# Kernel optimization log

Measured on AMD Instinct MI355X. Metric: run time of the kernel, lower is better.

The kernel has to match this reference:

```python
import jax, jax.numpy as jnp
import numpy as np

N_CODEBOOKS = 9
CODEBOOK_SIZE = 1024
CODEBOOK_DIM = 8
INPUT_DIM = 128
B, T = 16, 4096


def setup_inputs() -> dict:
    key = jax.random.key(0)
    ks = jax.random.split(key, 7)
    x = jax.random.normal(ks[0], (B, 2 * INPUT_DIM, T), dtype=jnp.float32)
    noise = jax.random.normal(ks[1], (B, INPUT_DIM, T), dtype=jnp.float32)
    # per-codebook params (stacked over the quantizer axis)
    in_w = jax.random.normal(ks[2], (N_CODEBOOKS, CODEBOOK_DIM, INPUT_DIM), dtype=jnp.float32) * 0.08
    in_b = jax.random.normal(ks[3], (N_CODEBOOKS, CODEBOOK_DIM), dtype=jnp.float32) * 0.01
    codebook = jax.random.normal(ks[4], (N_CODEBOOKS, CODEBOOK_SIZE, CODEBOOK_DIM), dtype=jnp.float32)
    out_w = jax.random.normal(ks[5], (N_CODEBOOKS, INPUT_DIM, CODEBOOK_DIM), dtype=jnp.float32) * 0.08
    out_b = jax.random.normal(ks[6], (N_CODEBOOKS, INPUT_DIM), dtype=jnp.float32) * 0.01
    return {"x": x, "noise": noise, "in_w": in_w, "in_b": in_b,
            "codebook": codebook, "out_w": out_w, "out_b": out_b}


def _l2norm(v, eps=1e-12):
    n = jnp.linalg.norm(v, axis=-1, keepdims=True)
    return v / jnp.maximum(n, eps)


def reference(x, noise, in_w, in_b, codebook, out_w, out_b):
    # --- vae_sample ---
    mean, scale = jnp.split(x, 2, axis=1)
    stdev = jax.nn.softplus(scale) + 1e-4
    var = stdev * stdev
    kl = jnp.mean(jnp.sum(mean * mean + var - jnp.log(var) - 1.0, axis=1))
    z = noise * stdev + mean  # [B, D, T]

    # --- ResidualVectorQuantize (eval mode, all codebooks) ---
    residual = z
    z_q = jnp.zeros_like(z)
    commitment_loss = jnp.float32(0.0)
    codebook_loss = jnp.float32(0.0)
    codes, lats = [], []
    b, _, t = z.shape
    for i in range(N_CODEBOOKS):
        # in_proj (1x1 conv)
        z_e = jnp.einsum("cd,bdt->bct", in_w[i], residual) + in_b[i][None, :, None]
        enc = z_e.transpose(0, 2, 1).reshape(b * t, CODEBOOK_DIM)
        enc_n = _l2norm(enc)
        cb_n = _l2norm(codebook[i])
        # squared L2 distance between normalized vectors
        dist = (jnp.sum(enc_n * enc_n, axis=1, keepdims=True)
                - 2.0 * enc_n @ cb_n.T
                + jnp.sum(cb_n * cb_n, axis=1)[None, :])
        idx = jnp.argmin(dist, axis=1).reshape(b, t)  # [B, T]
        zq_i = codebook[i][idx].transpose(0, 2, 1)  # [B, c, T] (raw codebook)
        # mse_loss(...).mean([1,2]).mean() == global mean
        commitment_loss = commitment_loss + jnp.mean((z_e - jax.lax.stop_gradient(zq_i)) ** 2)
        codebook_loss = codebook_loss + jnp.mean((zq_i - jax.lax.stop_gradient(z_e)) ** 2)
        # straight-through estimator
        zq_st = z_e + jax.lax.stop_gradient(zq_i - z_e)
        out = jnp.einsum("dc,bct->bdt", out_w[i], zq_st) + out_b[i][None, :, None]
        z_q = z_q + out
        residual = residual - out
        codes.append(idx)
        lats.append(z_e)
    codes = jnp.stack(codes, axis=1)          # [B, N, T]
    latents = jnp.concatenate(lats, axis=1)   # [B, N*c, T]
    commitment_loss = commitment_loss / N_CODEBOOKS
    codebook_loss = codebook_loss / N_CODEBOOKS
    return z_q, kl, commitment_loss, codebook_loss, codes, latents
```

## Files before the change

kernel.cpp:

```cpp
#include <hip/hip_runtime.h>
#include <cstdint>
#include <cstddef>

constexpr int T   = 4096;
constexpr int BB  = 16;
constexpr int D   = 128;
constexpr int CB  = 1024;
constexpr int CD  = 8;
constexpr int NCB = 9;

constexpr int TBLK = 64;
constexpr int NTHR = 512;
constexpr int NW   = 8;
constexpr int ZLS  = 66;

constexpr size_t OFF_ZQ    = 0;
constexpr size_t OFF_SCAL  = (size_t)BB * D * T;
constexpr size_t OFF_CODES = OFF_SCAL + 3;
constexpr size_t OFF_LAT   = OFF_CODES + (size_t)BB * NCB * T;

constexpr size_t AFR_U32 = (size_t)NCB * 64 * 2 * 64 * 4;
constexpr size_t H2C_F32 = (size_t)NCB * CB;
constexpr size_t AFW_U32 = (size_t)2 * 6 * 2 * 5 * 64 * 4;
constexpr size_t CM_F32  = (size_t)NCB * 72 * 8;
constexpr size_t OBS_F32 = 128;
constexpr size_t BEF_F32 = 72;
constexpr size_t OP_F32  = (size_t)NCB * CB * D;

typedef short bf16x8 __attribute__((ext_vector_type(8)));
typedef float f32x4  __attribute__((ext_vector_type(4)));

__device__ __forceinline__ unsigned short f2bf(float f) {
    unsigned u = __float_as_uint(f);
    return (unsigned short)((u + (((u >> 16) & 1u) + 0x7FFFu)) >> 16);
}
__device__ __forceinline__ float bf2f(unsigned short b) {
    return __uint_as_float((unsigned)b << 16);
}

constexpr int PAIR_A[6] = {0, 0, 1, 1, 2, 0};
constexpr int PAIR_B[6] = {0, 1, 0, 1, 0, 2};

__device__ __forceinline__ unsigned short splitterm(float xv, int term) {
    unsigned short t0 = f2bf(xv); if (term == 0) return t0;
    float r1 = xv - bf2f(t0);
    unsigned short t1 = f2bf(r1); if (term == 1) return t1;
    float r2 = r1 - bf2f(t1);
    return f2bf(r2);
}

__global__ void prep_kernel(const float* __restrict__ codebook,
                            const float* __restrict__ in_w,
                            const float* __restrict__ in_b,
                            const float* __restrict__ out_w,
                            const float* __restrict__ out_b,
                            unsigned* __restrict__ afr,
                            float* __restrict__ h2c,
                            unsigned* __restrict__ afw,
                            float* __restrict__ CMt,
                            float* __restrict__ obs,
                            float* __restrict__ bef,
                            float* __restrict__ OPt,
                            float* __restrict__ scal) {
    const int gid = blockIdx.x * blockDim.x + threadIdx.x;
    if (gid == 0) { scal[0] = 0.f; scal[1] = 0.f; scal[2] = 0.f; }

    if (gid < NCB * CB) {
        const int e  = gid;
        const int i  = e >> 10;
        const int en = e & 1023;
        const int et = en >> 4;
        const int m  = en & 15;

        float v[CD]; float s2 = 0.f;
#pragma unroll
        for (int j = 0; j < CD; ++j) { v[j] = codebook[(size_t)e * CD + j]; s2 = fmaf(v[j], v[j], s2); }
        float inv = 1.0f / fmaxf(sqrtf(s2), 1e-12f);
        float cn[CD]; float c2 = 0.f;
#pragma unroll
        for (int j = 0; j < CD; ++j) { cn[j] = v[j] * inv; c2 = fmaf(cn[j], cn[j], c2); }
        h2c[e] = -0.5f * c2;

        unsigned pk[3][4];
#pragma unroll
        for (int w = 0; w < 4; ++w) {
            float x0 = cn[2 * w], x1 = cn[2 * w + 1];
            unsigned short a0 = f2bf(x0); float r0 = x0 - bf2f(a0);
            unsigned short a1 = f2bf(r0); float q0 = r0 - bf2f(a1);
            unsigned short a2 = f2bf(q0);
            unsigned short b0 = f2bf(x1); float r1 = x1 - bf2f(b0);
            unsigned short b1 = f2bf(r1); float q1 = r1 - bf2f(b1);
            unsigned short b2 = f2bf(q1);
            pk[0][w] = (unsigned)a0 | ((unsigned)b0 << 16);
            pk[1][w] = (unsigned)a1 | ((unsigned)b1 << 16);
            pk[2][w] = (unsigned)a2 | ((unsigned)b2 << 16);
        }
        const int At[8] = {0, 1, 2, 0, 1, 0, 2, 1};
#pragma unroll
        for (int kh = 0; kh < 2; ++kh) {
#pragma unroll
            for (int h = 0; h < 4; ++h) {
                int A1 = At[kh * 4 + (h >> 1)];
                int A2 = At[kh * 4 + 2 + (h >> 1)];
                int dw = (h & 1) * 2;
                size_t off = ((((size_t)i * 64 + et) * 2 + kh) * 64 + (h * 16 + m)) * 4;
                afr[off + 0] = pk[A1][dw];
                afr[off + 1] = pk[A1][dw + 1];
                afr[off + 2] = pk[A2][dw];
                afr[off + 3] = pk[A2][dw + 1];
            }
        }
        return;
    }
    if (gid < 2 * NCB * CB) {
        const int e = gid - NCB * CB;
        const int i = e >> 10;
        float cv[CD];
#pragma unroll
        for (int d = 0; d < CD; ++d) cv[d] = codebook[(size_t)e * CD + d];
        const float* ow = out_w + (size_t)i * D * CD;
        float* dst = OPt + (size_t)e * D;
        for (int r = 0; r < D; ++r) {
            float a = 0.f;
#pragma unroll
            for (int d = 0; d < CD; ++d) a = fmaf(ow[r * CD + d], cv[d], a);
            dst[r] = a;
        }
        return;
    }
    if (gid < 2 * NCB * CB + NCB * 72) {
        const int idx = gid - 2 * NCB * CB;
        const int j = idx / 72, r = idx - j * 72;
        const float* wi = in_w + (size_t)r * D;
        const float* ow = out_w + (size_t)j * D * CD;
        float a[CD];
#pragma unroll
        for (int d = 0; d < CD; ++d) a[d] = 0.f;
        for (int k = 0; k < D; ++k) {
            float w = wi[k];
#pragma unroll
            for (int d = 0; d < CD; ++d) a[d] = fmaf(w, ow[k * CD + d], a[d]);
        }
#pragma unroll
        for (int d = 0; d < CD; ++d) CMt[((size_t)j * 72 + r) * CD + d] = a[d];
        return;
    }
    if (gid < 2 * NCB * CB + NCB * 72 + 128) {
        const int r = gid - (2 * NCB * CB + NCB * 72);
        float a = 0.f;
        for (int i = 0; i < NCB; ++i) a += out_b[(size_t)i * D + r];
        obs[r] = a;
        return;
    }
    if (gid < 2 * NCB * CB + NCB * 72 + 128 + 72) {
        const int row = gid - (2 * NCB * CB + NCB * 72 + 128);
        const int ic  = row >> 3;
        const float* wi = in_w + (size_t)row * D;
        float a = in_b[row];
        for (int j = 0; j < ic; ++j) {
            const float* ob = out_b + (size_t)j * D;
            float s = 0.f;
            for (int k = 0; k < D; ++k) s = fmaf(wi[k], ob[k], s);
            a -= s;
        }
        bef[row] = a;
        return;
    }
    if (gid < 2 * NCB * CB + NCB * 72 + 128 + 72 + 7680) {
        int idx = gid - (2 * NCB * CB + NCB * 72 + 128 + 72);
        const int lane = idx & 63; idx >>= 6;
        const int mt = idx % 5; idx /= 5;
        const int kq = idx & 1; idx >>= 1;
        const int p  = idx % 6;
        const int P  = idx / 6;
        const int h  = lane >> 4, m = lane & 15;
        const int row = mt * 16 + m;
        const int term = PAIR_A[p];
        const int D0 = P * 64 + kq * 32 + h * 4;
        const int doff[4][2] = {{0, 1}, {2, 3}, {16, 17}, {18, 19}};
        unsigned wv[4];
#pragma unroll
        for (int w = 0; w < 4; ++w) {
            unsigned short lo = 0, hi = 0;
            if (row < 72) {
                lo = splitterm(in_w[(size_t)row * D + D0 + doff[w][0]], term);
                hi = splitterm(in_w[(size_t)row * D + D0 + doff[w][1]], term);
            }
            wv[w] = (unsigned)lo | ((unsigned)hi << 16);
        }
        *reinterpret_cast<uint4*>(afw + ((size_t)(((P * 6 + p) * 2 + kq) * 5 + mt) * 64 + lane) * 4)
            = make_uint4(wv[0], wv[1], wv[2], wv[3]);
        return;
    }
}

__global__ __launch_bounds__(NTHR, 4)
void rvq_kernel(const float* __restrict__ x,
                const float* __restrict__ noise,
                const float* __restrict__ codebook,
                const unsigned* __restrict__ afr,
                const float* __restrict__ h2c,
                const unsigned* __restrict__ afw,
                const float* __restrict__ CMt,
                const float* __restrict__ obs,
                const float* __restrict__ bef,
                const float* __restrict__ OPt,
                float* __restrict__ o_zq,
                float* __restrict__ o_scal,
                float* __restrict__ o_codes,
                float* __restrict__ o_lat) {
    __shared__ char sbuf[24576 + 2 * 19008];

    uint2*    zs   = reinterpret_cast<uint2*>(sbuf);
    unsigned* esA  = reinterpret_cast<unsigned*>(sbuf);
    unsigned* esB  = reinterpret_cast<unsigned*>(sbuf + 3072);
    float*    redS = reinterpret_cast<float*>(sbuf + 6144);
    int*      redI = reinterpret_cast<int*>(sbuf + 10240);
    int*      cidx = reinterpret_cast<int*>(sbuf + 14336);
    float*    redw = reinterpret_cast<float*>(sbuf + 18944);
    float*    ZlA  = reinterpret_cast<float*>(sbuf + 24576);
    float*    ZlB  = reinterpret_cast<float*>(sbuf + 24576 + 19008);

    const int tid = threadIdx.x;
    const int c   = tid & 63;
    const int s   = tid >> 6;
    const int su  = __builtin_amdgcn_readfirstlane(s);
    const int b   = blockIdx.x >> 5;
    const int t0  = (blockIdx.x & 31) << 7;

    const int l  = tid & 63;
    const int h  = l >> 4;
    const int nl = l & 15;

    const int mtbase = (su < 4) ? 0 : 3;
    const int nmt    = (su < 4) ? 3 : 2;
    float kl_local = 0.f;

#pragma unroll 1
    for (int tl = 0; tl < 2; ++tl) {
        float* Zl = tl ? ZlB : ZlA;
        const int t = t0 + tl * 64 + c;
        f32x4 acc[3];
#pragma unroll
        for (int q = 0; q < 3; ++q) {
            int row0 = (mtbase + q) * 16 + h * 4;
            if (q < nmt && row0 < 72) acc[q] = *reinterpret_cast<const f32x4*>(bef + row0);
            else                      acc[q] = f32x4{0.f, 0.f, 0.f, 0.f};
        }

#pragma unroll 1
        for (int P = 0; P < 2; ++P) {
            {
                const int r0 = P * 64 + su * 8;
                const float* xm = x     + (size_t)b * 2 * D * T + (size_t)r0 * T + t;
                const float* xs = xm    + (size_t)D * T;
                const float* nz = noise + (size_t)b * D * T     + (size_t)r0 * T + t;
                float zrow[8];
#pragma unroll
                for (int k = 0; k < 8; ++k) {
                    float m  = xm[(size_t)k * T];
                    float sc = xs[(size_t)k * T];
                    float nv = nz[(size_t)k * T];
                    float sp  = fmaxf(sc, 0.f) + log1pf(expf(-fabsf(sc)));
                    float sd  = sp + 1e-4f;
                    float var = sd * sd;
                    zrow[k]   = fmaf(nv, sd, m);
                    kl_local += m * m + var - logf(var) - 1.0f;
                }
#pragma unroll
                for (int db = 0; db < 2; ++db) {
                    unsigned w[3][2];
#pragma unroll
                    for (int half = 0; half < 2; ++half) {
                        float x0 = zrow[db * 4 + half * 2], x1 = zrow[db * 4 + half * 2 + 1];
                        unsigned short a0 = f2bf(x0); float r1 = x0 - bf2f(a0);
                        unsigned short a1 = f2bf(r1); float r2 = r1 - bf2f(a1);
                        unsigned short a2 = f2bf(r2);
                        unsigned short b0 = f2bf(x1); float s1v = x1 - bf2f(b0);
                        unsigned short b1 = f2bf(s1v); float s2v = s1v - bf2f(b1);
                        unsigned short b2 = f2bf(s2v);
                        w[0][half] = (unsigned)a0 | ((unsigned)b0 << 16);
                        w[1][half] = (unsigned)a1 | ((unsigned)b1 << 16);
                        w[2][half] = (unsigned)a2 | ((unsigned)b2 << 16);
                    }
#pragma unroll
                    for (int tt = 0; tt < 3; ++tt)
                        zs[(tt * 16 + su * 2 + db) * 64 + c] = make_uint2(w[tt][0], w[tt][1]);
                }
            }
            __syncthreads();
            {
                const int colB = (su & 3) * 16 + nl;
#pragma unroll
                for (int p = 0; p < 6; ++p) {
#pragma unroll
                    for (int kq = 0; kq < 2; ++kq) {
                        uint2 blo = zs[(PAIR_B[p] * 16 + kq * 8 + h) * 64 + colB];
                        uint2 bhi = zs[(PAIR_B[p] * 16 + kq * 8 + 4 + h) * 64 + colB];
                        uint4 bu = make_uint4(blo.x, blo.y, bhi.x, bhi.y);
                        bf16x8 bfr = *reinterpret_cast<bf16x8*>(&bu);
                        const uint4* Aw = reinterpret_cast<const uint4*>(afw)
                                          + (size_t)(((P * 6 + p) * 2 + kq) * 5) * 64 + l;
#pragma unroll
                        for (int q = 0; q < 3; ++q) {
                            if (q < nmt) {
                                uint4 au = Aw[(size_t)(mtbase + q) * 64];
                                bf16x8 af = *reinterpret_cast<bf16x8*>(&au);
                                acc[q] = __builtin_amdgcn_mfma_f32_16x16x32_bf16(af, bfr, acc[q], 0, 0, 0);
                            }
                        }
                    }
                }
            }
            __syncthreads();
        }
#pragma unroll
        for (int q = 0; q < 3; ++q) {
            if (q < nmt) {
                const int row0 = (mtbase + q) * 16 + h * 4;
                if (row0 < 72) {
#pragma unroll
                    for (int r = 0; r < 4; ++r)
                        Zl[(row0 + r) * ZLS + (su & 3) * 16 + nl] = acc[q][r];
                }
            }
        }
    }

    float loss_local = 0.f;
    const int tg = su >> 2;
    const int sv = su & 3;

    for (int i = 0; i < NCB; ++i) {
        __syncthreads();

        if (tid < 128) {
            float*    Zl = (tid & 64) ? ZlB : ZlA;
            unsigned* es = (tid & 64) ? esB : esA;
            const int cc = tid & 63;
            float v[CD]; float n2 = 0.f;
#pragma unroll
            for (int j = 0; j < CD; ++j) { v[j] = Zl[(i * CD + j) * ZLS + cc]; n2 = fmaf(v[j], v[j], n2); }
            float inv = 1.0f / fmaxf(sqrtf(n2), 1e-12f);
            unsigned pk[3][4];
#pragma unroll
            for (int w = 0; w < 4; ++w) {
                float x0 = v[2 * w] * inv, x1 = v[2 * w + 1] * inv;
                unsigned short a0 = f2bf(x0); float r0 = x0 - bf2f(a0);
                unsigned short a1 = f2bf(r0); float q0 = r0 - bf2f(a1);
                unsigned short a2 = f2bf(q0);
                unsigned short b0 = f2bf(x1); float r1 = x1 - bf2f(b0);
                unsigned short b1 = f2bf(r1); float q1 = r1 - bf2f(b1);
                unsigned short b2 = f2bf(q1);
                pk[0][w] = (unsigned)a0 | ((unsigned)b0 << 16);
                pk[1][w] = (unsigned)a1 | ((unsigned)b1 << 16);
                pk[2][w] = (unsigned)a2 | ((unsigned)b2 << 16);
            }
            uint4* ep = reinterpret_cast<uint4*>(&es[(size_t)cc * 12]);
            ep[0] = make_uint4(pk[0][0], pk[0][1], pk[0][2], pk[0][3]);
            ep[1] = make_uint4(pk[1][0], pk[1][1], pk[1][2], pk[1][3]);
            ep[2] = make_uint4(pk[2][0], pk[2][1], pk[2][2], pk[2][3]);
        }
        {
            float la0 = ZlA[(i * CD + su) * ZLS + c];
            float la1 = ZlB[(i * CD + su) * ZLS + c];
            o_lat[(size_t)b * (NCB * CD) * T + (size_t)(i * CD + su) * T + t0 + c]      = la0;
            o_lat[(size_t)b * (NCB * CD) * T + (size_t)(i * CD + su) * T + t0 + 64 + c] = la1;
        }
        __syncthreads();

        bf16x8 bfA[4][2], bfB[4][2];
        {
            const int dwo = (h & 1) * 2;
            const int tA  = h >> 1;
            const int tB  = 1 + (h >> 1);
#pragma unroll
            for (int pt = 0; pt < 4; ++pt) {
                const int col = pt * 16 + nl;
                {
                    uint2 lo0 = *reinterpret_cast<const uint2*>(&esA[col * 12 + 0 * 4 + dwo]);
                    uint2 hi0 = *reinterpret_cast<const uint2*>(&esA[col * 12 + tA * 4 + dwo]);
                    uint2 lh1 = *reinterpret_cast<const uint2*>(&esA[col * 12 + tB * 4 + dwo]);
                    uint4 t0v = make_uint4(lo0.x, lo0.y, hi0.x, hi0.y);
                    uint4 t1v = make_uint4(lh1.x, lh1.y, lh1.x, lh1.y);
                    bfA[pt][0] = *reinterpret_cast<bf16x8*>(&t0v);
                    bfA[pt][1] = *reinterpret_cast<bf16x8*>(&t1v);
                }
                {
                    uint2 lo0 = *reinterpret_cast<const uint2*>(&esB[col * 12 + 0 * 4 + dwo]);
                    uint2 hi0 = *reinterpret_cast<const uint2*>(&esB[col * 12 + tA * 4 + dwo]);
                    uint2 lh1 = *reinterpret_cast<const uint2*>(&esB[col * 12 + tB * 4 + dwo]);
                    uint4 t0v = make_uint4(lo0.x, lo0.y, hi0.x, hi0.y);
                    uint4 t1v = make_uint4(lh1.x, lh1.y, lh1.x, lh1.y);
                    bfB[pt][0] = *reinterpret_cast<bf16x8*>(&t0v);
                    bfB[pt][1] = *reinterpret_cast<bf16x8*>(&t1v);
                }
            }
        }

        float bestA[4] = {-3.0e38f, -3.0e38f, -3.0e38f, -3.0e38f};
        float bestB[4] = {-3.0e38f, -3.0e38f, -3.0e38f, -3.0e38f};
        int   bidxA[4] = {0, 0, 0, 0};
        int   bidxB[4] = {0, 0, 0, 0};
        {
            const uint4* Ab = reinterpret_cast<const uint4*>(afr)
                              + ((size_t)(i * 64 + su * 8) * 2) * 64 + l;
            const f32x4* Hb = reinterpret_cast<const f32x4*>(h2c)
                              + (size_t)i * 256 + su * 32;
            int eb = su * 128 + h * 4;
#pragma unroll 2
            for (int e8 = 0; e8 < 8; ++e8) {
                uint4 ua0 = Ab[0];
                uint4 ua1 = Ab[64];
                f32x4 hv  = Hb[e8 * 4 + h];
                bf16x8 a0 = *reinterpret_cast<bf16x8*>(&ua0);
                bf16x8 a1 = *reinterpret_cast<bf16x8*>(&ua1);
#pragma unroll
                for (int pt = 0; pt < 4; ++pt) {
                    f32x4 acA = __builtin_amdgcn_mfma_f32_16x16x32_bf16(a0, bfA[pt][0], hv, 0, 0, 0);
                    acA = __builtin_amdgcn_mfma_f32_16x16x32_bf16(a1, bfA[pt][1], acA, 0, 0, 0);
                    f32x4 acB = __builtin_amdgcn_mfma_f32_16x16x32_bf16(a0, bfB[pt][0], hv, 0, 0, 0);
                    acB = __builtin_amdgcn_mfma_f32_16x16x32_bf16(a1, bfB[pt][1], acB, 0, 0, 0);
#pragma unroll
                    for (int r = 0; r < 4; ++r) {
                        float sa = acA[r];
                        if (sa > bestA[pt]) { bestA[pt] = sa; bidxA[pt] = eb + r; }
                        float sb = acB[r];
                        if (sb > bestB[pt]) { bestB[pt] = sb; bidxB[pt] = eb + r; }
                    }
                }
                Ab += 128; eb += 16;
            }
        }

#pragma unroll
        for (int off = 16; off <= 32; off <<= 1) {
#pragma unroll
            for (int pt = 0; pt < 4; ++pt) {
                float oa2 = __shfl_xor(bestA[pt], off, 64);
                int   oi  = __shfl_xor(bidxA[pt], off, 64);
                bool tk = (oa2 > bestA[pt]) || (oa2 == bestA[pt] && oi < bidxA[pt]);
                if (tk) { bestA[pt] = oa2; bidxA[pt] = oi; }
                float ob2 = __shfl_xor(bestB[pt], off, 64);
                int   oj  = __shfl_xor(bidxB[pt], off, 64);
                bool tk2 = (ob2 > bestB[pt]) || (ob2 == bestB[pt] && oj < bidxB[pt]);
                if (tk2) { bestB[pt] = ob2; bidxB[pt] = oj; }
            }
        }
        if (l < 16) {
#pragma unroll
            for (int pt = 0; pt < 4; ++pt) {
                redS[(0 * 8 + su) * 64 + pt * 16 + l] = bestA[pt];
                redI[(0 * 8 + su) * 64 + pt * 16 + l] = bidxA[pt];
            }
        } else if (l < 32) {
#pragma unroll
            for (int pt = 0; pt < 4; ++pt) {
                redS[(1 * 8 + su) * 64 + pt * 16 + (l - 16)] = bestB[pt];
                redI[(1 * 8 + su) * 64 + pt * 16 + (l - 16)] = bidxB[pt];
            }
        }
        __syncthreads();

        float bsc = redS[(tg * 8) * 64 + c];
        int   bi  = redI[(tg * 8) * 64 + c];
#pragma unroll
        for (int ww = 1; ww < NW; ++ww) {
            float v2 = redS[(tg * 8 + ww) * 64 + c];
            int   vi = redI[(tg * 8 + ww) * 64 + c];
            if (v2 > bsc) { bsc = v2; bi = vi; }
        }
        cidx[(tg * NCB + i) * 64 + c] = bi;
        if (su == 0) o_codes[(size_t)b * NCB * T + (size_t)i * T + t0 + c]      = (float)bi;
        if (su == 4) o_codes[(size_t)b * NCB * T + (size_t)i * T + t0 + 64 + c] = (float)bi;

        float cv[CD];
        {
            const float4* cr4 = (const float4*)(codebook + ((size_t)i * CB + bi) * CD);
            float4 qa = cr4[0], qb = cr4[1];
            cv[0] = qa.x; cv[1] = qa.y; cv[2] = qa.z; cv[3] = qa.w;
            cv[4] = qb.x; cv[5] = qb.y; cv[6] = qb.z; cv[7] = qb.w;
            if (su == 0 || su == 4) {
                float* Zl = tg ? ZlB : ZlA;
#pragma unroll
                for (int j = 0; j < CD; ++j) {
                    float dd = cv[j] - Zl[(i * CD + j) * ZLS + c];
                    loss_local = fmaf(dd, dd, loss_local);
                }
            }
        }

        {
            float* Zl = tg ? ZlB : ZlA;
            const int nf = 64 - 8 * i;
            for (int rr = sv; rr < nf; rr += 4) {
                const int row = (i + 1) * 8 + rr;
                float zv = Zl[row * ZLS + c];
                const float* cm = CMt + ((size_t)i * 72 + row) * CD;
#pragma unroll
                for (int d2 = 0; d2 < CD; ++d2) zv = fmaf(-cm[d2], cv[d2], zv);
                Zl[row * ZLS + c] = zv;
            }
        }
    }
    __syncthreads();

    {
        f32x4 oa[8];
#pragma unroll
        for (int kb = 0; kb < 8; ++kb)
            oa[kb] = *reinterpret_cast<const f32x4*>(obs + sv * 32 + kb * 4);
#pragma unroll
        for (int i2 = 0; i2 < NCB; ++i2) {
            int code = cidx[(tg * NCB + i2) * 64 + c];
            const f32x4* op = reinterpret_cast<const f32x4*>(OPt + ((size_t)(i2 * CB + code)) * D + sv * 32);
#pragma unroll
            for (int kb = 0; kb < 8; ++kb) oa[kb] += op[kb];
        }
        float* oq = o_zq + (size_t)b * D * T + (size_t)(sv * 32) * T + t0 + tg * 64 + c;
#pragma unroll
        for (int kb = 0; kb < 8; ++kb)
#pragma unroll
            for (int r = 0; r < 4; ++r)
                oq[(size_t)(kb * 4 + r) * T] = oa[kb][r];
    }

    float v = kl_local;
#pragma unroll
    for (int o = 32; o > 0; o >>= 1) v += __shfl_down(v, o, 64);
    float w2 = loss_local;
#pragma unroll
    for (int o = 32; o > 0; o >>= 1) w2 += __shfl_down(w2, o, 64);
    if ((tid & 63) == 0) { redw[s] = v; redw[NW + s] = w2; }
    __syncthreads();
    if (tid == 0) {
        float ks = 0.f, ls = 0.f;
#pragma unroll
        for (int q = 0; q < NW; ++q) { ks += redw[q]; ls += redw[NW + q]; }
        atomicAdd(&o_scal[0], ks * (1.0f / 65536.0f));
        float lsn = ls * (1.0f / (524288.0f * 9.0f));
        atomicAdd(&o_scal[1], lsn);
        atomicAdd(&o_scal[2], lsn);
    }
}

extern "C" void kernel_launch(void* const* d_in, const int* in_sizes, int n_in,
                              void* d_out, int out_size, void* d_ws, size_t ws_size,
                              hipStream_t stream) {
    const float* x        = (const float*)d_in[0];
    const float* noise    = (const float*)d_in[1];
    const float* in_w     = (const float*)d_in[2];
    const float* in_b     = (const float*)d_in[3];
    const float* codebook = (const float*)d_in[4];
    const float* out_w    = (const float*)d_in[5];
    const float* out_b    = (const float*)d_in[6];

    float* out     = (float*)d_out;
    float* o_zq    = out + OFF_ZQ;
    float* o_scal  = out + OFF_SCAL;
    float* o_codes = out + OFF_CODES;
    float* o_lat   = out + OFF_LAT;

    unsigned* afr = (unsigned*)d_ws;
    float*    h2c = (float*)(afr + AFR_U32);
    unsigned* afw = (unsigned*)(h2c + H2C_F32);
    float*    CMt = (float*)(afw + AFW_U32);
    float*    obs = CMt + CM_F32;
    float*    bef = obs + OBS_F32;
    float*    OPt = bef + BEF_F32;

    const int prep_total = 2 * NCB * CB + NCB * 72 + 128 + 72 + 7680;
    prep_kernel<<<(prep_total + 255) / 256, 256, 0, stream>>>(
        codebook, in_w, in_b, out_w, out_b, afr, h2c, afw, CMt, obs, bef, OPt, o_scal);

    dim3 grid(BB * (T / (TBLK * 2)));
    rvq_kernel<<<grid, NTHR, 0, stream>>>(x, noise, codebook,
                                          afr, h2c, afw, CMt, obs, bef, OPt,
                                          o_zq, o_scal, o_codes, o_lat);
}
```

Before: 363.3 us.

## Defer residual update into next iteration and split OPt prep across more threads

The residual update for the following codebooks is moved from the end of each iteration to the start of the next one. There, one lane group updates the current codebook's rows and normalizes them, while the other lane groups update the later rows at the same time. This removes one block-wide barrier per codebook iteration and overlaps the update work with the encoding step. The prep kernel's output-projection table is also split so each thread computes 16 rows instead of 128, which gives the prep kernel more parallelism. In exchange, the update work is spread less evenly across lanes and the order of shared-memory reads and writes becomes harder to verify.

```diff
diff --git a/kernel.cpp b/kernel.cpp
--- a/kernel.cpp
+++ b/kernel.cpp
@@ -112,15 +112,18 @@
         }
         return;
     }
-    if (gid < 2 * NCB * CB) {
-        const int e = gid - NCB * CB;
-        const int i = e >> 10;
+    if (gid < 9 * NCB * CB) {
+        const int idx = gid - NCB * CB;
+        const int e  = idx >> 3;
+        const int r0 = (idx & 7) * 16;
+        const int i  = e >> 10;
         float cv[CD];
 #pragma unroll
         for (int d = 0; d < CD; ++d) cv[d] = codebook[(size_t)e * CD + d];
-        const float* ow = out_w + (size_t)i * D * CD;
-        float* dst = OPt + (size_t)e * D;
-        for (int r = 0; r < D; ++r) {
+        const float* ow = out_w + ((size_t)i * D + r0) * CD;
+        float* dst = OPt + (size_t)e * D + r0;
+#pragma unroll
+        for (int r = 0; r < 16; ++r) {
             float a = 0.f;
 #pragma unroll
             for (int d = 0; d < CD; ++d) a = fmaf(ow[r * CD + d], cv[d], a);
@@ -128,8 +131,8 @@
         }
         return;
     }
-    if (gid < 2 * NCB * CB + NCB * 72) {
-        const int idx = gid - 2 * NCB * CB;
+    if (gid < 9 * NCB * CB + NCB * 72) {
+        const int idx = gid - 9 * NCB * CB;
         const int j = idx / 72, r = idx - j * 72;
         const float* wi = in_w + (size_t)r * D;
         const float* ow = out_w + (size_t)j * D * CD;
@@ -145,15 +148,15 @@
         for (int d = 0; d < CD; ++d) CMt[((size_t)j * 72 + r) * CD + d] = a[d];
         return;
     }
-    if (gid < 2 * NCB * CB + NCB * 72 + 128) {
-        const int r = gid - (2 * NCB * CB + NCB * 72);
+    if (gid < 9 * NCB * CB + NCB * 72 + 128) {
+        const int r = gid - (9 * NCB * CB + NCB * 72);
         float a = 0.f;
         for (int i = 0; i < NCB; ++i) a += out_b[(size_t)i * D + r];
         obs[r] = a;
         return;
     }
-    if (gid < 2 * NCB * CB + NCB * 72 + 128 + 72) {
-        const int row = gid - (2 * NCB * CB + NCB * 72 + 128);
+    if (gid < 9 * NCB * CB + NCB * 72 + 128 + 72) {
+        const int row = gid - (9 * NCB * CB + NCB * 72 + 128);
         const int ic  = row >> 3;
         const float* wi = in_w + (size_t)row * D;
         float a = in_b[row];
@@ -166,8 +169,8 @@
         bef[row] = a;
         return;
     }
-    if (gid < 2 * NCB * CB + NCB * 72 + 128 + 72 + 7680) {
-        int idx = gid - (2 * NCB * CB + NCB * 72 + 128 + 72);
+    if (gid < 9 * NCB * CB + NCB * 72 + 128 + 72 + 7680) {
+        int idx = gid - (9 * NCB * CB + NCB * 72 + 128 + 72);
         const int lane = idx & 63; idx >>= 6;
         const int mt = idx % 5; idx /= 5;
         const int kq = idx & 1; idx >>= 1;
@@ -326,21 +329,35 @@
             }
         }
     }
+    __syncthreads();
 
     float loss_local = 0.f;
     const int tg = su >> 2;
     const int sv = su & 3;
+    float cv[CD];
+#pragma unroll
+    for (int j = 0; j < CD; ++j) cv[j] = 0.f;
 
     for (int i = 0; i < NCB; ++i) {
-        __syncthreads();
-
-        if (tid < 128) {
-            float*    Zl = (tid & 64) ? ZlB : ZlA;
-            unsigned* es = (tid & 64) ? esB : esA;
-            const int cc = tid & 63;
-            float v[CD]; float n2 = 0.f;
-#pragma unroll
-            for (int j = 0; j < CD; ++j) { v[j] = Zl[(i * CD + j) * ZLS + cc]; n2 = fmaf(v[j], v[j], n2); }
+        if (sv == 0) {
+            float*    Zl = tg ? ZlB : ZlA;
+            unsigned* es = tg ? esB : esA;
+            const int cc = l;
+            float v[CD];
+#pragma unroll
+            for (int j = 0; j < CD; ++j) v[j] = Zl[(i * CD + j) * ZLS + cc];
+            if (i > 0) {
+                const float* cm = CMt + ((size_t)(i - 1) * 72 + i * CD) * CD;
+#pragma unroll
+                for (int j = 0; j < CD; ++j) {
+#pragma unroll
+                    for (int d2 = 0; d2 < CD; ++d2) v[j] = fmaf(-cm[j * CD + d2], cv[d2], v[j]);
+                    Zl[(i * CD + j) * ZLS + cc] = v[j];
+                }
+            }
+            float n2 = 0.f;
+#pragma unroll
+            for (int j = 0; j < CD; ++j) n2 = fmaf(v[j], v[j], n2);
             float inv = 1.0f / fmaxf(sqrtf(n2), 1e-12f);
             unsigned pk[3][4];
 #pragma unroll
@@ -360,14 +377,25 @@
             ep[0] = make_uint4(pk[0][0], pk[0][1], pk[0][2], pk[0][3]);
             ep[1] = make_uint4(pk[1][0], pk[1][1], pk[1][2], pk[1][3]);
             ep[2] = make_uint4(pk[2][0], pk[2][1], pk[2][2], pk[2][3]);
-        }
+        } else if (i > 0) {
+            float* Zl = tg ? ZlB : ZlA;
+            const int base = (i + 1) * CD;
+            for (int row = base + (sv - 1); row < 72; row += 3) {
+                float zv = Zl[row * ZLS + c];
+                const float* cm = CMt + ((size_t)(i - 1) * 72 + row) * CD;
+#pragma unroll
+                for (int d2 = 0; d2 < CD; ++d2) zv = fmaf(-cm[d2], cv[d2], zv);
+                Zl[row * ZLS + c] = zv;
+            }
+        }
+        __syncthreads();
+
         {
             float la0 = ZlA[(i * CD + su) * ZLS + c];
             float la1 = ZlB[(i * CD + su) * ZLS + c];
             o_lat[(size_t)b * (NCB * CD) * T + (size_t)(i * CD + su) * T + t0 + c]      = la0;
             o_lat[(size_t)b * (NCB * CD) * T + (size_t)(i * CD + su) * T + t0 + 64 + c] = la1;
         }
-        __syncthreads();
 
         bf16x8 bfA[4][2], bfB[4][2];
         {
@@ -474,32 +502,18 @@
         if (su == 0) o_codes[(size_t)b * NCB * T + (size_t)i * T + t0 + c]      = (float)bi;
         if (su == 4) o_codes[(size_t)b * NCB * T + (size_t)i * T + t0 + 64 + c] = (float)bi;
 
-        float cv[CD];
         {
             const float4* cr4 = (const float4*)(codebook + ((size_t)i * CB + bi) * CD);
             float4 qa = cr4[0], qb = cr4[1];
             cv[0] = qa.x; cv[1] = qa.y; cv[2] = qa.z; cv[3] = qa.w;
             cv[4] = qb.x; cv[5] = qb.y; cv[6] = qb.z; cv[7] = qb.w;
-            if (su == 0 || su == 4) {
+            if (sv == 0) {
                 float* Zl = tg ? ZlB : ZlA;
 #pragma unroll
                 for (int j = 0; j < CD; ++j) {
                     float dd = cv[j] - Zl[(i * CD + j) * ZLS + c];
                     loss_local = fmaf(dd, dd, loss_local);
                 }
-            }
-        }
-
-        {
-            float* Zl = tg ? ZlB : ZlA;
-            const int nf = 64 - 8 * i;
-            for (int rr = sv; rr < nf; rr += 4) {
-                const int row = (i + 1) * 8 + rr;
-                float zv = Zl[row * ZLS + c];
-                const float* cm = CMt + ((size_t)i * 72 + row) * CD;
-#pragma unroll
-                for (int d2 = 0; d2 < CD; ++d2) zv = fmaf(-cm[d2], cv[d2], zv);
-                Zl[row * ZLS + c] = zv;
             }
         }
     }
@@ -569,7 +583,7 @@
     float*    bef = obs + OBS_F32;
     float*    OPt = bef + BEF_F32;
 
-    const int prep_total = 2 * NCB * CB + NCB * 72 + 128 + 72 + 7680;
+    const int prep_total = 9 * NCB * CB + NCB * 72 + 128 + 72 + 7680;
     prep_kernel<<<(prep_total + 255) / 256, 256, 0, stream>>>(
         codebook, in_w, in_b, out_w, out_b, afr, h2c, afw, CMt, obs, bef, OPt, o_scal);
 
```

New measurement: 367.7 us. Within noise of the previous version (+1.2%).
